# Optimization experiments

Hardware: AMD Instinct MI355X
Metric: run time of the kernel (lower is better)

The kernel has to match this reference:

```python
import jax, jax.numpy as jnp
import numpy as np

SIDES, LAYERS, NH = 2, 2, 2
DEPTH, B = 7, 8
NPT = (3 ** DEPTH - 1) // 2  # 1093 nodes per perfect ternary tree
N = B * NPT                  # 8744
E, H = 256, 512
NUM_USERS, NUM_POIS, NUM_CATS, NUM_COOS, TMAX = 2000, 5000, 300, 50, 600
FUSE = NUM_POIS + NUM_CATS + NUM_COOS


def setup_inputs() -> dict:
    key = jax.random.key(0)
    cnt = [0]
    def nk():
        cnt[0] += 1
        return jax.random.fold_in(key, cnt[0])
    def rn(*s):
        return jax.random.normal(nk(), s, jnp.float32) * 0.02
    inp = dict(
        user_ids=jax.random.randint(nk(), (SIDES, N), 0, NUM_USERS, jnp.int32),
        feat_ids=jax.random.randint(nk(), (SIDES, N), 0, FUSE, jnp.int32),
        time_ids=jax.random.randint(nk(), (SIDES, N), 0, TMAX, jnp.int32),
        mask=jnp.ones((SIDES, N), jnp.int32),
        depth=DEPTH, n_trees=B,
        user_emb=rn(SIDES, NUM_USERS, 128), fuse_emb=rn(SIDES, FUSE, 128),
        time_pe=rn(SIDES, TMAX, E),
        Wf=rn(SIDES, H, E), bf=jnp.zeros((SIDES, H)),
        Wiou=rn(SIDES, 3 * H, E), Uiou=rn(SIDES, 3 * H, 3 * H), biou=jnp.zeros((SIDES, 3 * H)),
        attn_in_w=rn(SIDES, LAYERS, 3 * H, H), attn_in_b=jnp.zeros((SIDES, LAYERS, 3 * H)),
        attn_out_w=rn(SIDES, LAYERS, H, H), attn_out_b=jnp.zeros((SIDES, LAYERS, H)),
        ff1_w=rn(SIDES, LAYERS, H, H), ff1_b=jnp.zeros((SIDES, LAYERS, H)),
        ff2_w=rn(SIDES, LAYERS, H, H), ff2_b=jnp.zeros((SIDES, LAYERS, H)),
        ln1_w=jnp.ones((SIDES, LAYERS, H)), ln1_b=jnp.zeros((SIDES, LAYERS, H)),
        ln2_w=jnp.ones((SIDES, LAYERS, H)), ln2_b=jnp.zeros((SIDES, LAYERS, H)),
        dec_poi_w=rn(SIDES, NUM_POIS, H), dec_poi_b=jnp.zeros((SIDES, NUM_POIS)),
        dec_cat_w=rn(SIDES, NUM_CATS, H), dec_cat_b=jnp.zeros((SIDES, NUM_CATS)),
        dec_coo_w=rn(SIDES, NUM_COOS, H), dec_coo_b=jnp.zeros((SIDES, NUM_COOS)),
        cat2poi_w=rn(SIDES, NUM_POIS, NUM_CATS), cat2poi_b=jnp.zeros((SIDES, NUM_POIS)),
        coo2poi_w=rn(SIDES, NUM_POIS, NUM_COOS), coo2poi_b=jnp.zeros((SIDES, NUM_POIS)),
        mtl=jnp.ones((SIDES, 3)),
        c0=(jax.random.uniform(nk(), (SIDES, N, H), jnp.float32) * 2.0 - 1.0) * 0.025,
    )
    return inp


def _ln(x, w, b, eps=1e-5):
    m = x.mean(-1, keepdims=True)
    v = ((x - m) ** 2).mean(-1, keepdims=True)
    return (x - m) / jnp.sqrt(v + eps) * w + b


def _mha(x, iw, ib, ow, ob):
    M, S, Hd = x.shape
    q, k, v = jnp.split(x @ iw.T + ib, 3, -1)
    hd = Hd // NH
    def rs(t):
        return t.reshape(M, S, NH, hd).transpose(0, 2, 1, 3)
    q, k, v = rs(q), rs(k), rs(v)
    att = jax.nn.softmax((q * (hd ** -0.5)) @ k.transpose(0, 1, 3, 2), -1)
    o = (att @ v).transpose(0, 2, 1, 3).reshape(M, S, Hd)
    return o @ ow.T + ob


def _enc(x, iw, ib, ow, ob, f1w, f1b, f2w, f2b, l1w, l1b, l2w, l2b):
    # post-norm TransformerEncoderLayer, relu, eval mode (no dropout)
    x = _ln(x + _mha(x, iw, ib, ow, ob), l1w, l1b)
    return _ln(x + (jax.nn.relu(x @ f1w.T + f1b) @ f2w.T + f2b), l2w, l2b)


def _forward(user_ids, feat_ids, time_ids, mask, depth, n_trees,
             user_emb, fuse_emb, time_pe, Wf, bf, Wiou, Uiou, biou,
             attn_in_w, attn_in_b, attn_out_w, attn_out_b,
             ff1_w, ff1_b, ff2_w, ff2_b, ln1_w, ln1_b, ln2_w, ln2_b,
             dec_poi_w, dec_poi_b, dec_cat_w, dec_cat_b, dec_coo_w, dec_coo_b,
             cat2poi_w, cat2poi_b, coo2poi_w, coo2poi_b, mtl, c0):
    Hd = Wf.shape[1]
    npt = (3 ** depth - 1) // 2
    Bt = n_trees
    offs = [(3 ** l - 1) // 2 for l in range(depth)]
    outs = []
    for s in range(SIDES):
        m = mask[s]
        uid, fid, tid = user_ids[s] * m, feat_ids[s] * m, time_ids[s] * m
        emb = jnp.concatenate([user_emb[s][uid], fuse_emb[s][fid]], -1) + 0.5 * time_pe[s][tid]
        mf = m.astype(emb.dtype)[:, None]
        x = (emb * mf).reshape(Bt, npt, -1)              # masked node features
        iou0 = ((emb @ Wiou[s].T) * mf).reshape(Bt, npt, 3 * Hd)  # leaf iou init
        c0s = c0[s].reshape(Bt, npt, Hd)
        h = jnp.zeros((Bt, npt, Hd), emb.dtype)
        c = jnp.zeros((Bt, npt, Hd), emb.dtype)
        for l in range(depth - 1, -1, -1):  # bottom-up topo propagation, level-major layout
            st, n = offs[l], 3 ** l
            if l == depth - 1:  # leaves: no reduce, apply with initial iou and c
                iou = iou0[:, st:st + n]
                cpre = c0s[:, st:st + n]
            else:
                cs = offs[l + 1]
                hch = h[:, cs:cs + 3 * n].reshape(Bt * n, 3, Hd)   # mailbox h_child
                cch = c[:, cs:cs + 3 * n].reshape(Bt, n, 3, Hd)    # mailbox c_child
                z = hch
                for L in range(LAYERS):
                    z = _enc(z, attn_in_w[s, L], attn_in_b[s, L], attn_out_w[s, L], attn_out_b[s, L],
                             ff1_w[s, L], ff1_b[s, L], ff2_w[s, L], ff2_b[s, L],
                             ln1_w[s, L], ln1_b[s, L], ln2_w[s, L], ln2_b[s, L])
                hc = z.reshape(Bt, n, 3 * Hd)
                xl = x[:, st:st + n]
                Wx = xl @ Wf[s].T
                f = jax.nn.sigmoid(jnp.concatenate([Wx] * 3, -1) + hc + jnp.tile(bf[s], 3))
                iou = xl @ Wiou[s].T + hc @ Uiou[s].T + biou[s]
                cpre = jnp.sum(f.reshape(Bt, n, 3, Hd) * cch, axis=2)
            i, o, u = jnp.split(iou, 3, -1)
            cn = jax.nn.sigmoid(i) * jnp.tanh(u) + cpre
            hn = jax.nn.sigmoid(o) * jnp.tanh(cn)
            h = h.at[:, st:st + n].set(hn)
            c = c.at[:, st:st + n].set(cn)
        hN = h.reshape(-1, Hd)
        poi = hN @ dec_poi_w[s].T + dec_poi_b[s]
        cat = hN @ dec_cat_w[s].T + dec_cat_b[s]
        coo = hN @ dec_coo_w[s].T + dec_coo_b[s]
        p = mtl[s]
        poi_mt = (0.5 * jnp.exp(-p[0]) * poi + p[0]
                  + 0.5 * jnp.exp(-p[1]) * (cat @ cat2poi_w[s].T + cat2poi_b[s]) + p[1]
                  + 0.5 * jnp.exp(-p[2]) * (coo @ coo2poi_w[s].T + coo2poi_b[s]) + p[2])
        outs += [poi_mt, cat, coo]
    return tuple(outs)


def reference(user_ids, feat_ids, time_ids, mask, depth, n_trees,
              user_emb, fuse_emb, time_pe, Wf, bf, Wiou, Uiou, biou,
              attn_in_w, attn_in_b, attn_out_w, attn_out_b,
              ff1_w, ff1_b, ff2_w, ff2_b, ln1_w, ln1_b, ln2_w, ln2_b,
              dec_poi_w, dec_poi_b, dec_cat_w, dec_cat_b, dec_coo_w, dec_coo_b,
              cat2poi_w, cat2poi_b, coo2poi_w, coo2poi_b, mtl, c0):
    return _forward(user_ids, feat_ids, time_ids, mask, depth, n_trees,
                    user_emb, fuse_emb, time_pe, Wf, bf, Wiou, Uiou, biou,
                    attn_in_w, attn_in_b, attn_out_w, attn_out_b,
                    ff1_w, ff1_b, ff2_w, ff2_b, ln1_w, ln1_b, ln2_w, ln2_b,
                    dec_poi_w, dec_poi_b, dec_cat_w, dec_cat_b, dec_coo_w, dec_coo_b,
                    cat2poi_w, cat2poi_b, coo2poi_w, coo2poi_b, mtl, c0)
```

## Files before the change

### kernel.cpp

```cpp
#include <hip/hip_runtime.h>
#include <math.h>

#define SIDES 2
#define LAYERS 2
#define NTREE 8
#define NPT 1093
#define NN (NTREE*NPT)
#define EE 256
#define HH 512
#define NUSERS 2000
#define NPOI 5000
#define NCAT 300
#define NCOO 50
#define FUSEN 5350
#define TMAXN 600
#define TOKMAX 5832
#define PARMAX 1944

constexpr long OUT_S   = 46780400L;
constexpr long CAT_OFF = 43720000L;
constexpr long COO_OFF = 46343200L;

constexpr long H_S    = (long)NN*HH;
constexpr long X_S    = (long)NN*EE;
constexpr long Z_S    = (long)TOKMAX*HH;
constexpr long QKV_S  = (long)TOKMAX*3*HH;
constexpr long WXI_S  = (long)PARMAX*2048;
constexpr long WEFF_S = (long)NPOI*HH;

typedef __attribute__((ext_vector_type(8))) short  bf16x8;
typedef __attribute__((ext_vector_type(8))) ushort u16x8;
typedef __attribute__((ext_vector_type(4))) ushort u16x4;
typedef __attribute__((ext_vector_type(4))) float  f32x4;

__device__ __forceinline__ float sigm(float x){ return 1.f/(1.f+expf(-x)); }
__device__ __forceinline__ ushort f2b(float f){
  union { float f; unsigned u; } v; v.f = f;
  return (ushort)((v.u + 0x7fffu + ((v.u >> 16) & 1u)) >> 16);
}
__device__ __forceinline__ float b2f(ushort u){
  union { unsigned u; float f; } v; v.u = (unsigned)u << 16; return v.f;
}

__global__ void mcvt_k(ushort* d0, const float* s0, long n0,
                       ushort* d1, const float* s1, long n1,
                       ushort* d2, const float* s2, long n2,
                       ushort* d3, const float* s3, long n3,
                       ushort* d4, const float* s4, long n4,
                       ushort* d5, const float* s5, long n5){
  long g4 = (long)blockIdx.x*blockDim.x + threadIdx.x;
  long i = g4*4;
  ushort* d; const float* s; long off;
  if      (i < n0){ d=d0; s=s0; off=i; }
  else if ((i-=n0) < n1){ d=d1; s=s1; off=i; }
  else if ((i-=n1) < n2){ d=d2; s=s2; off=i; }
  else if ((i-=n2) < n3){ d=d3; s=s3; off=i; }
  else if ((i-=n3) < n4){ d=d4; s=s4; off=i; }
  else if ((i-=n4) < n5){ d=d5; s=s5; off=i; }
  else return;
  f32x4 v = *(const f32x4*)(s + off);
  *(u16x4*)(d + off) = (u16x4){f2b(v[0]), f2b(v[1]), f2b(v[2]), f2b(v[3])};
}

__global__ void wcomb_k(ushort* __restrict__ dst, const float* __restrict__ Wf,
                        const float* __restrict__ Wiou, const float* __restrict__ Uiou){
  int s = blockIdx.z; int row = blockIdx.x; int col = blockIdx.y*256 + threadIdx.x;
  float v;
  if (row < 512) v = (col < 256) ? Wf[((long)s*512 + row)*256 + col] : 0.f;
  else {
    int r = row - 512;
    v = (col < 256) ? Wiou[((long)s*1536 + r)*256 + col]
                    : Uiou[((long)s*1536 + r)*1536 + (col-256)];
  }
  dst[(long)s*2048*1792 + (long)row*1792 + col] = f2b(v);
}

__global__ void bcomb_k(float* __restrict__ dst, const float* __restrict__ biou){
  int s = blockIdx.z; int c = blockIdx.x*256 + threadIdx.x;
  dst[(long)s*2048 + c] = (c < 512) ? 0.f : biou[(long)s*1536 + (c-512)];
}

__global__ void padcvt_k(ushort* __restrict__ dst, const float* __restrict__ src,
                         int rows, int scols, int dcols){
  int s = blockIdx.z; int r = blockIdx.x; int c = blockIdx.y*256 + threadIdx.x;
  if (c >= dcols) return;
  float v = (c < scols) ? src[((long)s*rows + r)*scols + c] : 0.f;
  dst[((long)s*rows + r)*dcols + c] = f2b(v);
}

__global__ void tpcvt_k(ushort* __restrict__ dst, const float* __restrict__ src,
                        int srows, int dcols){
  int s = blockIdx.z; int h = blockIdx.x; int c = threadIdx.x;
  float v = (c < srows) ? src[((long)s*srows + c)*512 + h] : 0.f;
  dst[((long)s*512 + h)*dcols + c] = f2b(v);
}

__global__ void weffinit_k(ushort* __restrict__ dst, const float* __restrict__ poi_w,
                           const float* __restrict__ mtl){
  int s = blockIdx.z;
  long i = ((long)blockIdx.x*blockDim.x + threadIdx.x)*4;
  float a0 = 0.5f*expf(-mtl[(long)s*3]);
  f32x4 v = *(const f32x4*)(poi_w + (long)s*WEFF_S + i);
  *(u16x4*)(dst + (long)s*WEFF_S + i) =
      (u16x4){f2b(a0*v[0]), f2b(a0*v[1]), f2b(a0*v[2]), f2b(a0*v[3])};
}

__global__ void beff_k(float* __restrict__ beff, const float* __restrict__ poi_b,
                       const float* __restrict__ cat_b, const float* __restrict__ c2p_w,
                       const float* __restrict__ c2p_b, const float* __restrict__ coo_b,
                       const float* __restrict__ o2p_w, const float* __restrict__ o2p_b,
                       const float* __restrict__ mtl){
  int s = blockIdx.z;
  int n = blockIdx.x*blockDim.x + threadIdx.x;
  if (n >= NPOI) return;
  const float* mt = mtl + (long)s*3;
  float a0 = 0.5f*expf(-mt[0]), a1 = 0.5f*expf(-mt[1]), a2 = 0.5f*expf(-mt[2]);
  float acc1 = 0.f, acc2 = 0.f;
  for (int c = 0; c < NCAT; c++)
    acc1 += cat_b[(long)s*NCAT + c] * c2p_w[((long)s*NPOI + n)*NCAT + c];
  for (int c = 0; c < NCOO; c++)
    acc2 += coo_b[(long)s*NCOO + c] * o2p_w[((long)s*NPOI + n)*NCOO + c];
  beff[(long)s*NPOI + n] = a0*poi_b[(long)s*NPOI + n]
      + a1*(acc1 + c2p_b[(long)s*NPOI + n]) + a2*(acc2 + o2p_b[(long)s*NPOI + n])
      + mt[0] + mt[1] + mt[2];
}

__global__ void embed_k(const int* __restrict__ uid, const int* __restrict__ fid,
                        const int* __restrict__ tid, const int* __restrict__ mask,
                        const float* __restrict__ uemb, const float* __restrict__ femb,
                        const float* __restrict__ tpe, ushort* __restrict__ X){
  int s = blockIdx.z; long i = blockIdx.x; int d = threadIdx.x;
  int m = mask[(long)s*NN + i];
  int u = uid[(long)s*NN + i]*m, f = fid[(long)s*NN + i]*m, t = tid[(long)s*NN + i]*m;
  float e = (d < 128) ? uemb[((long)s*NUSERS + u)*128 + d]
                      : femb[((long)s*FUSEN + f)*128 + (d-128)];
  e += 0.5f * tpe[((long)s*TMAXN + t)*256 + d];
  X[(long)s*X_S + i*EE + d] = f2b(e * (float)m);
}

template<int MODE, bool OBF>
__global__ void __launch_bounds__(256)
mgemm_k(const ushort* __restrict__ A1, long lda1, long sA1,
        const ushort* __restrict__ A2, long lda2, long sA2,
        int kSplit, int mapN, int mapOff,
        const ushort* __restrict__ Wt, long ldw, long sW,
        const float* __restrict__ bias, long sB,
        void* __restrict__ Cv, long ldc, long sC,
        int M, int Nc, int K, int nbx,
        const float* __restrict__ mtl, int mtlIdx){
  int s = blockIdx.z;
  A1 += (long)s*sA1; A2 += (long)s*sA2; Wt += (long)s*sW;
  if (bias) bias += (long)s*sB;

  int flat = blockIdx.x, nwg = gridDim.x;
  int xcd = flat & 7, q = nwg >> 3, r8 = nwg & 7;
  int nf = (xcd < r8 ? xcd*(q+1) : r8*(q+1) + (xcd - r8)*q) + (flat >> 3);
  int bx = nf % nbx, by = nf / nbx;
  int m0 = by*128, n0 = bx*128;

  __shared__ ushort As[128*64];
  __shared__ ushort Ws[128*64];

  int tid = threadIdx.x;
  int lane = tid & 63, wave = tid >> 6;
  int wr = wave >> 1, wc = wave & 1;
  int fr = lane & 15, kc = lane >> 4;

  int baseRow = tid >> 3;
  int c16 = tid & 7;
  int col8 = c16*8;
  int swz = (baseRow & 7) << 4;

  long gA1[4], gA2[4], gW[4];
  int wbyte[4];
  #pragma unroll
  for (int c = 0; c < 4; c++){
    int row = baseRow + c*32;
    int ra = m0 + row; if (ra > M-1) ra = M-1;
    gA2[c] = ra;
    if (mapN > 0){ int tr = ra / mapN; gA1[c] = (long)(tr*NPT + mapOff + (ra - tr*mapN)); }
    else gA1[c] = ra;
    int rw = n0 + row; if (rw > Nc-1) rw = Nc-1;
    gW[c] = rw;
    wbyte[c] = row*128 + ((c16*16) ^ swz);
  }

  u16x8 rA[4], rW[4];
  {
    bool u1 = (0 < kSplit);
    const ushort* asrc = u1 ? A1 : A2;
    long ld = u1 ? lda1 : lda2;
    const long* g = u1 ? gA1 : gA2;
    #pragma unroll
    for (int c = 0; c < 4; c++){
      rA[c] = *(const u16x8*)(asrc + g[c]*ld + col8);
      rW[c] = *(const u16x8*)(Wt + gW[c]*ldw + col8);
    }
  }

  f32x4 acc[4][4];
  #pragma unroll
  for (int i = 0; i < 4; i++)
    #pragma unroll
    for (int j = 0; j < 4; j++) acc[i][j] = (f32x4){0.f,0.f,0.f,0.f};

  for (int k0 = 0; k0 < K; k0 += 64){
    #pragma unroll
    for (int c = 0; c < 4; c++){
      *(u16x8*)((char*)As + wbyte[c]) = rA[c];
      *(u16x8*)((char*)Ws + wbyte[c]) = rW[c];
    }
    __syncthreads();
    int kn = k0 + 64;
    if (kn < K){
      bool u1 = (kn < kSplit);
      const ushort* asrc = u1 ? A1 : A2;
      long ld = u1 ? lda1 : lda2;
      const long* g = u1 ? gA1 : gA2;
      long colb = u1 ? (long)kn : (long)(kn - kSplit);
      #pragma unroll
      for (int c = 0; c < 4; c++){
        rA[c] = *(const u16x8*)(asrc + g[c]*ld + colb + col8);
        rW[c] = *(const u16x8*)(Wt + gW[c]*ldw + kn + col8);
      }
    }
    #pragma unroll
    for (int h = 0; h < 2; h++){
      bf16x8 af[4], bw[4];
      #pragma unroll
      for (int i = 0; i < 4; i++){
        int row = wr*64 + i*16 + fr;
        int byo = row*128 + ((h*64 + kc*16) ^ ((row & 7) << 4));
        af[i] = *(const bf16x8*)((const char*)As + byo);
      }
      #pragma unroll
      for (int j = 0; j < 4; j++){
        int row = wc*64 + j*16 + fr;
        int byo = row*128 + ((h*64 + kc*16) ^ ((row & 7) << 4));
        bw[j] = *(const bf16x8*)((const char*)Ws + byo);
      }
      #pragma unroll
      for (int i = 0; i < 4; i++)
        #pragma unroll
        for (int j = 0; j < 4; j++)
          acc[i][j] = __builtin_amdgcn_mfma_f32_16x16x32_bf16(bw[j], af[i], acc[i][j], 0, 0, 0);
    }
    __syncthreads();
  }

  float alpha = 1.f;
  if (MODE == 4) alpha = 0.5f*expf(-mtl[(long)s*3 + mtlIdx]);
  int ccol = lane & 15, cr4 = (lane >> 4)*4;
  bool vecN = ((Nc & 3) == 0);
  float* Cf = (float*)Cv + (long)s*sC;
  ushort* Cb = (ushort*)Cv + (long)s*sC;
  #pragma unroll
  for (int i = 0; i < 4; i++){
    int gm = m0 + wr*64 + i*16 + ccol;
    if (gm >= M) continue;
    long rowoff = (long)gm*ldc;
    #pragma unroll
    for (int j = 0; j < 4; j++){
      int gn0 = n0 + wc*64 + j*16 + cr4;
      if (gn0 >= Nc) continue;
      f32x4 v = acc[i][j];
      if (MODE != 4 && bias){ f32x4 bv = *(const f32x4*)&bias[gn0]; v += bv; }
      if (MODE == 1){ v = (f32x4){fmaxf(v[0],0.f),fmaxf(v[1],0.f),fmaxf(v[2],0.f),fmaxf(v[3],0.f)}; }
      if (OBF){
        u16x4* cp = (u16x4*)&Cb[rowoff + gn0];
        if (MODE == 4){
          u16x4 o = *cp;
          *cp = (u16x4){f2b(b2f(o[0]) + alpha*v[0]), f2b(b2f(o[1]) + alpha*v[1]),
                        f2b(b2f(o[2]) + alpha*v[2]), f2b(b2f(o[3]) + alpha*v[3])};
        } else {
          *cp = (u16x4){f2b(v[0]), f2b(v[1]), f2b(v[2]), f2b(v[3])};
        }
      } else {
        if (vecN){
          f32x4* cp = (f32x4*)&Cf[rowoff + gn0];
          if (MODE == 4){ f32x4 o = *cp; *cp = o + alpha*v; }
          else *cp = v;
        } else {
          #pragma unroll
          for (int r = 0; r < 4; r++){
            int gn = gn0 + r; if (gn >= Nc) continue;
            if (MODE == 4) Cf[rowoff + gn] += alpha*v[r];
            else Cf[rowoff + gn] = v[r];
          }
        }
      }
    }
  }
}

__global__ void attn_k(const ushort* __restrict__ qkv, ushort* __restrict__ o){
  int s = blockIdx.z, m = blockIdx.x, h = blockIdx.y;
  const ushort* base = qkv + (long)s*QKV_S + (long)m*3*1536 + (long)h*256;
  int t = threadIdx.x;
  float q[3], k[3], v[3];
  #pragma unroll
  for (int i = 0; i < 3; i++){
    q[i] = b2f(base[(long)i*1536 + t]);
    k[i] = b2f(base[(long)i*1536 + 512 + t]);
    v[i] = b2f(base[(long)i*1536 + 1024 + t]);
  }
  __shared__ float sm[4];
  __shared__ float att[9];
  #pragma unroll
  for (int i = 0; i < 3; i++)
    #pragma unroll
    for (int j = 0; j < 3; j++){
      float p = q[i]*k[j];
      for (int off = 32; off; off >>= 1) p += __shfl_down(p, off);
      __syncthreads();
      if ((t & 63) == 0) sm[t >> 6] = p;
      __syncthreads();
      if (t == 0) att[i*3 + j] = (sm[0]+sm[1]+sm[2]+sm[3]) * 0.0625f;
    }
  __syncthreads();
  if (t < 3){
    float a = att[t*3], b = att[t*3+1], c = att[t*3+2];
    float mx = fmaxf(a, fmaxf(b, c));
    a = expf(a-mx); b = expf(b-mx); c = expf(c-mx);
    float inv = 1.f/(a+b+c);
    att[t*3] = a*inv; att[t*3+1] = b*inv; att[t*3+2] = c*inv;
  }
  __syncthreads();
  ushort* ob = o + (long)s*Z_S + (long)m*3*512 + (long)h*256;
  #pragma unroll
  for (int i = 0; i < 3; i++)
    ob[(long)i*512 + t] = f2b(att[i*3]*v[0] + att[i*3+1]*v[1] + att[i*3+2]*v[2]);
}

__global__ void add_ln_k(ushort* __restrict__ zout, long sZ,
                         const ushort* __restrict__ res, long sR, int mapN, int mapOff,
                         const ushort* __restrict__ tb, long sT,
                         const float* __restrict__ w, const float* __restrict__ b, long wstr){
  int s = blockIdx.z; int r = blockIdx.x;
  int g = r;
  if (mapN > 0){ int tr = r / mapN; g = tr*NPT + mapOff + (r - tr*mapN); }
  const ushort* rr = res + (long)s*sR + (long)g*HH;
  const ushort* tr_ = tb + (long)s*sT + (long)r*HH;
  const float* wr = w + (long)s*wstr;
  const float* br = b + (long)s*wstr;
  int d0 = threadIdx.x, d1 = threadIdx.x + 256;
  float x0 = b2f(rr[d0]) + b2f(tr_[d0]), x1 = b2f(rr[d1]) + b2f(tr_[d1]);
  __shared__ float sm[4];
  float tsum = x0 + x1;
  for (int off = 32; off; off >>= 1) tsum += __shfl_down(tsum, off);
  if ((threadIdx.x & 63) == 0) sm[threadIdx.x >> 6] = tsum;
  __syncthreads();
  float mean = (sm[0]+sm[1]+sm[2]+sm[3]) * (1.f/512.f);
  float e0 = x0 - mean, e1 = x1 - mean;
  float vs = e0*e0 + e1*e1;
  __syncthreads();
  for (int off = 32; off; off >>= 1) vs += __shfl_down(vs, off);
  if ((threadIdx.x & 63) == 0) sm[threadIdx.x >> 6] = vs;
  __syncthreads();
  float var = (sm[0]+sm[1]+sm[2]+sm[3]) * (1.f/512.f);
  float inv = 1.f/sqrtf(var + 1e-5f);
  ushort* zr = zout + (long)s*sZ + (long)r*HH;
  zr[d0] = f2b(e0*inv*wr[d0] + br[d0]);
  zr[d1] = f2b(e1*inv*wr[d1] + br[d1]);
}

__global__ void leaf_k(const ushort* __restrict__ iou, const float* __restrict__ c0,
                       ushort* __restrict__ hbuf, float* __restrict__ cbuf){
  int s = blockIdx.z, p = blockIdx.x;
  int tree = p / 729, j = p - tree*729;
  long row = (long)(tree*NPT + 364 + j)*HH;
  const ushort* iour = iou + (long)s*QKV_S + (long)p*1536;
  const float* c0r = c0 + (long)s*H_S + row;
  for (int d = threadIdx.x; d < HH; d += 256){
    float cn = sigm(b2f(iour[d])) * tanhf(b2f(iour[1024 + d])) + c0r[d];
    float hn = sigm(b2f(iour[512 + d])) * tanhf(cn);
    hbuf[(long)s*H_S + row + d] = f2b(hn);
    cbuf[(long)s*H_S + row + d] = cn;
  }
}

__global__ void combine_k(const ushort* __restrict__ wxiou, const ushort* __restrict__ z,
                          const float* __restrict__ bfv, const float* __restrict__ cbuf,
                          ushort* __restrict__ hbuf, float* __restrict__ cout,
                          int n, int st, int cs){
  int s = blockIdx.z, p = blockIdx.x;
  int tree = p / n, j = p - tree*n;
  const ushort* wr_ = wxiou + (long)s*WXI_S + (long)p*2048;
  const ushort* zr  = z + (long)s*Z_S + (long)p*1536;
  const float* bfr  = bfv + (long)s*HH;
  const float* cch  = cbuf + (long)s*H_S + (long)(tree*NPT + cs + 3*j)*HH;
  long orow = (long)s*H_S + (long)(tree*NPT + st + j)*HH;
  for (int d = threadIdx.x; d < HH; d += 256){
    float wv = b2f(wr_[d]) + bfr[d];
    float cpre = 0.f;
    #pragma unroll
    for (int ch = 0; ch < 3; ch++){
      float fg = sigm(wv + b2f(zr[ch*512 + d]));
      cpre += fg * cch[ch*512 + d];
    }
    float iv = b2f(wr_[512 + d]), ov = b2f(wr_[1024 + d]), uv = b2f(wr_[1536 + d]);
    float cn = sigm(iv)*tanhf(uv) + cpre;
    float hn = sigm(ov)*tanhf(cn);
    hbuf[orow + d] = f2b(hn);
    cout[orow + d] = cn;
  }
}

#define GEMM(MODE, OBF, A1, LDA1, SA1, A2, LDA2, SA2, KSPL, MAPN, MAPOFF, WT, LDW, SW, \
             BI, SB, CC, LDC, SC, M, NC, K)                                            \
  do { int nbx_ = ((NC)+127)/128, nby_ = ((M)+127)/128;                                \
    mgemm_k<MODE, OBF><<<dim3(nbx_*nby_, 1, SIDES), 256, 0, stream>>>(                 \
      A1, LDA1, SA1, A2, LDA2, SA2, KSPL, MAPN, MAPOFF, WT, LDW, SW, BI, SB,           \
      CC, LDC, SC, M, NC, K, nbx_, mtl, 0); } while(0)
#define GEMM4(OBF, A1, LDA1, SA1, WT, LDW, SW, CC, LDC, SC, M, NC, K, IDX)             \
  do { int nbx_ = ((NC)+127)/128, nby_ = ((M)+127)/128;                                \
    mgemm_k<4, OBF><<<dim3(nbx_*nby_, 1, SIDES), 256, 0, stream>>>(                    \
      A1, LDA1, SA1, A1, LDA1, SA1, K, 0, 0, WT, LDW, SW, (const float*)nullptr, 0L,   \
      CC, LDC, SC, M, NC, K, nbx_, mtl, IDX); } while(0)

extern "C" void kernel_launch(void* const* d_in, const int* in_sizes, int n_in,
                              void* d_out, int out_size, void* d_ws, size_t ws_size,
                              hipStream_t stream){
  (void)in_sizes; (void)n_in; (void)out_size; (void)ws_size;
  const int*   user_ids  = (const int*)d_in[0];
  const int*   feat_ids  = (const int*)d_in[1];
  const int*   time_ids  = (const int*)d_in[2];
  const int*   mask      = (const int*)d_in[3];
  const float* user_emb  = (const float*)d_in[6];
  const float* fuse_emb  = (const float*)d_in[7];
  const float* time_pe   = (const float*)d_in[8];
  const float* Wf        = (const float*)d_in[9];
  const float* bf        = (const float*)d_in[10];
  const float* Wiou      = (const float*)d_in[11];
  const float* Uiou      = (const float*)d_in[12];
  const float* biou      = (const float*)d_in[13];
  const float* attn_in_w = (const float*)d_in[14];
  const float* attn_in_b = (const float*)d_in[15];
  const float* attn_out_w= (const float*)d_in[16];
  const float* attn_out_b= (const float*)d_in[17];
  const float* ff1_w     = (const float*)d_in[18];
  const float* ff1_b     = (const float*)d_in[19];
  const float* ff2_w     = (const float*)d_in[20];
  const float* ff2_b     = (const float*)d_in[21];
  const float* ln1_w     = (const float*)d_in[22];
  const float* ln1_b     = (const float*)d_in[23];
  const float* ln2_w     = (const float*)d_in[24];
  const float* ln2_b     = (const float*)d_in[25];
  const float* dec_poi_w = (const float*)d_in[26];
  const float* dec_poi_b = (const float*)d_in[27];
  const float* dec_cat_w = (const float*)d_in[28];
  const float* dec_cat_b = (const float*)d_in[29];
  const float* dec_coo_w = (const float*)d_in[30];
  const float* dec_coo_b = (const float*)d_in[31];
  const float* cat2poi_w = (const float*)d_in[32];
  const float* cat2poi_b = (const float*)d_in[33];
  const float* coo2poi_w = (const float*)d_in[34];
  const float* coo2poi_b = (const float*)d_in[35];
  const float* mtl       = (const float*)d_in[36];
  const float* c0        = (const float*)d_in[37];

  float* out = (float*)d_out;

  ushort* wsu = (ushort*)d_ws;
  ushort* Hb    = wsu;
  ushort* ainW  = Hb    + 2*H_S;
  ushort* aoutW = ainW  + (long)2*2*1536*512;
  ushort* f1W   = aoutW + (long)2*2*512*512;
  ushort* f2W   = f1W   + (long)2*2*512*512;
  ushort* wcomb = f2W   + (long)2*2*512*512;
  ushort* dcatW = wcomb + (long)2*2048*1792;
  ushort* dcooW = dcatW + (long)2*300*512;
  ushort* weffB = dcooW + (long)2*50*512;
  float*  bcomb = (float*)(weffB + (long)2*WEFF_S);
  float*  beff  = bcomb + 2*2048;

  float*  Cb   = out + OUT_S;
  ushort* osu  = (ushort*)(Cb + 2*H_S);
  ushort* QKV  = osu;
  ushort* Zb   = QKV  + 2*QKV_S;
  ushort* TMP  = Zb   + 2*Z_S;
  ushort* WXI  = TMP  + 2*Z_S;
  ushort* Xb   = WXI  + 2*WXI_S;
  ushort* c2pB = Xb   + 2*X_S;
  ushort* o2pB = c2pB + (long)2*5000*320;
  ushort* dctT = o2pB + (long)2*5000*64;
  ushort* dcoT = dctT + (long)2*512*320;

  {
    long n0 = (long)2*2*1536*512, n1 = (long)2*2*512*512, n2 = n1, n3 = n1;
    long n4 = (long)2*300*512, n5 = (long)2*50*512;
    long tot4 = (n0+n1+n2+n3+n4+n5)/4;
    mcvt_k<<<dim3((tot4+255)/256), 256, 0, stream>>>(
        ainW, attn_in_w, n0, aoutW, attn_out_w, n1, f1W, ff1_w, n2,
        f2W, ff2_w, n3, dcatW, dec_cat_w, n4, dcooW, dec_coo_w, n5);
  }
  wcomb_k<<<dim3(2048, 7, SIDES), 256, 0, stream>>>(wcomb, Wf, Wiou, Uiou);
  bcomb_k<<<dim3(8, 1, SIDES), 256, 0, stream>>>(bcomb, biou);
  padcvt_k<<<dim3(5000, 2, SIDES), 256, 0, stream>>>(c2pB, cat2poi_w, 5000, 300, 320);
  padcvt_k<<<dim3(5000, 1, SIDES), 256, 0, stream>>>(o2pB, coo2poi_w, 5000, 50, 64);
  tpcvt_k<<<dim3(512, 1, SIDES), 320, 0, stream>>>(dctT, dec_cat_w, 300, 320);
  tpcvt_k<<<dim3(512, 1, SIDES), 64, 0, stream>>>(dcoT, dec_coo_w, 50, 64);
  weffinit_k<<<dim3(2500, 1, SIDES), 256, 0, stream>>>(weffB, dec_poi_w, mtl);
  beff_k<<<dim3(20, 1, SIDES), 256, 0, stream>>>(beff, dec_poi_b, dec_cat_b,
       cat2poi_w, cat2poi_b, dec_coo_b, coo2poi_w, coo2poi_b, mtl);

  embed_k<<<dim3(NN, 1, SIDES), 256, 0, stream>>>(user_ids, feat_ids, time_ids, mask,
                                                  user_emb, fuse_emb, time_pe, Xb);

  GEMM(0, true, Xb, 256L, X_S, Xb, 256L, X_S, 256, 729, 364,
       wcomb + (long)512*1792, 1792L, (long)2048*1792,
       (const float*)nullptr, 0L, QKV, 1536L, QKV_S, 5832, 1536, 256);
  leaf_k<<<dim3(5832, 1, SIDES), 256, 0, stream>>>(QKV, c0, Hb, Cb);

  const int p3[7]   = {1,3,9,27,81,243,729};
  const int offs[7] = {0,1,4,13,40,121,364};

  for (int l = 5; l >= 0; l--){
    int n = p3[l], st = offs[l], cs = offs[l+1];
    int P = NTREE*n, T = 3*P;
    for (int L = 0; L < LAYERS; L++){
      const ushort* zin = (L == 0) ? Hb : Zb;
      long zld = 512, zs = (L == 0) ? H_S : Z_S;
      int mN = (L == 0) ? 3*n : 0, mO = (L == 0) ? cs : 0;
      GEMM(0, true, zin, zld, zs, zin, zld, zs, 512, mN, mO,
           ainW + (long)L*1536*512, 512L, (long)2*1536*512,
           attn_in_b + (long)L*1536, (long)LAYERS*1536, QKV, 1536L, QKV_S, T, 1536, 512);
      attn_k<<<dim3(P, 2, SIDES), 256, 0, stream>>>(QKV, TMP);
      GEMM(0, true, TMP, 512L, Z_S, TMP, 512L, Z_S, 512, 0, 0,
           aoutW + (long)L*512*512, 512L, (long)2*512*512,
           attn_out_b + (long)L*512, (long)LAYERS*512, QKV, 512L, QKV_S, T, 512, 512);
      add_ln_k<<<dim3(T, 1, SIDES), 256, 0, stream>>>(Zb, Z_S, zin, zs, mN, mO,
           QKV, QKV_S, ln1_w + (long)L*512, ln1_b + (long)L*512, (long)LAYERS*512);
      GEMM(1, true, Zb, 512L, Z_S, Zb, 512L, Z_S, 512, 0, 0,
           f1W + (long)L*512*512, 512L, (long)2*512*512,
           ff1_b + (long)L*512, (long)LAYERS*512, TMP, 512L, Z_S, T, 512, 512);
      GEMM(0, true, TMP, 512L, Z_S, TMP, 512L, Z_S, 512, 0, 0,
           f2W + (long)L*512*512, 512L, (long)2*512*512,
           ff2_b + (long)L*512, (long)LAYERS*512, QKV, 512L, QKV_S, T, 512, 512);
      add_ln_k<<<dim3(T, 1, SIDES), 256, 0, stream>>>(Zb, Z_S, Zb, Z_S, 0, 0,
           QKV, QKV_S, ln2_w + (long)L*512, ln2_b + (long)L*512, (long)LAYERS*512);
    }
    GEMM(0, true, Xb, 256L, X_S, Zb, 1536L, Z_S, 256, n, st,
         wcomb, 1792L, (long)2048*1792, bcomb, 2048L, WXI, 2048L, WXI_S, P, 2048, 1792);
    combine_k<<<dim3(P, 1, SIDES), 256, 0, stream>>>(WXI, Zb, bf, Cb, Hb, Cb, n, st, cs);
  }

  GEMM(0, false, Hb, 512L, H_S, Hb, 512L, H_S, 512, 0, 0,
       dcatW, 512L, (long)NCAT*512, dec_cat_b, (long)NCAT,
       out + CAT_OFF, (long)NCAT, OUT_S, NN, NCAT, 512);
  GEMM(0, false, Hb, 512L, H_S, Hb, 512L, H_S, 512, 0, 0,
       dcooW, 512L, (long)NCOO*512, dec_coo_b, (long)NCOO,
       out + COO_OFF, (long)NCOO, OUT_S, NN, NCOO, 512);

  GEMM4(true, c2pB, 320L, (long)5000*320, dctT, 320L, (long)512*320,
        weffB, 512L, WEFF_S, 5000, 512, 320, 1);
  GEMM4(true, o2pB, 64L, (long)5000*64, dcoT, 64L, (long)512*64,
        weffB, 512L, WEFF_S, 5000, 512, 64, 2);

  GEMM(0, false, Hb, 512L, H_S, Hb, 512L, H_S, 512, 0, 0,
       weffB, 512L, WEFF_S, beff, (long)NPOI,
       out, (long)NPOI, OUT_S, NN, NPOI, 512);
}
```

Measured before the change: 1.652 ms.

## Fuse prep kernels into one launch and make attention and LayerNorm wave-per-row

All weight conversion, padding, transpose, bias and embedding prep kernels are merged into a single prep_k launch, with blocks dispatched by index range. attn_k now gives each 64-lane wave one (sequence, head) pair with vectorized loads and xor-shuffle reductions, removing shared memory and __syncthreads. add_ln_k now handles one row per wave with 8-element vector loads and stores, so it launches four times fewer blocks. The aim is to cut launch overhead and synchronization in small kernels that run many times; the merged prep kernel has branchy block dispatch and some loops that leave lanes unevenly used.

```diff
diff --git a/kernel.cpp b/kernel.cpp
--- a/kernel.cpp
+++ b/kernel.cpp
@@ -42,100 +42,133 @@
   union { unsigned u; float f; } v; v.u = (unsigned)u << 16; return v.f;
 }
 
-__global__ void mcvt_k(ushort* d0, const float* s0, long n0,
-                       ushort* d1, const float* s1, long n1,
-                       ushort* d2, const float* s2, long n2,
-                       ushort* d3, const float* s3, long n3,
-                       ushort* d4, const float* s4, long n4,
-                       ushort* d5, const float* s5, long n5){
-  long g4 = (long)blockIdx.x*blockDim.x + threadIdx.x;
-  long i = g4*4;
-  ushort* d; const float* s; long off;
-  if      (i < n0){ d=d0; s=s0; off=i; }
-  else if ((i-=n0) < n1){ d=d1; s=s1; off=i; }
-  else if ((i-=n1) < n2){ d=d2; s=s2; off=i; }
-  else if ((i-=n2) < n3){ d=d3; s=s3; off=i; }
-  else if ((i-=n3) < n4){ d=d4; s=s4; off=i; }
-  else if ((i-=n4) < n5){ d=d5; s=s5; off=i; }
-  else return;
-  f32x4 v = *(const f32x4*)(s + off);
-  *(u16x4*)(d + off) = (u16x4){f2b(v[0]), f2b(v[1]), f2b(v[2]), f2b(v[3])};
-}
-
-__global__ void wcomb_k(ushort* __restrict__ dst, const float* __restrict__ Wf,
-                        const float* __restrict__ Wiou, const float* __restrict__ Uiou){
-  int s = blockIdx.z; int row = blockIdx.x; int col = blockIdx.y*256 + threadIdx.x;
-  float v;
-  if (row < 512) v = (col < 256) ? Wf[((long)s*512 + row)*256 + col] : 0.f;
-  else {
-    int r = row - 512;
-    v = (col < 256) ? Wiou[((long)s*1536 + r)*256 + col]
-                    : Uiou[((long)s*1536 + r)*1536 + (col-256)];
-  }
-  dst[(long)s*2048*1792 + (long)row*1792 + col] = f2b(v);
-}
-
-__global__ void bcomb_k(float* __restrict__ dst, const float* __restrict__ biou){
-  int s = blockIdx.z; int c = blockIdx.x*256 + threadIdx.x;
-  dst[(long)s*2048 + c] = (c < 512) ? 0.f : biou[(long)s*1536 + (c-512)];
-}
-
-__global__ void padcvt_k(ushort* __restrict__ dst, const float* __restrict__ src,
-                         int rows, int scols, int dcols){
-  int s = blockIdx.z; int r = blockIdx.x; int c = blockIdx.y*256 + threadIdx.x;
-  if (c >= dcols) return;
-  float v = (c < scols) ? src[((long)s*rows + r)*scols + c] : 0.f;
-  dst[((long)s*rows + r)*dcols + c] = f2b(v);
-}
-
-__global__ void tpcvt_k(ushort* __restrict__ dst, const float* __restrict__ src,
-                        int srows, int dcols){
-  int s = blockIdx.z; int h = blockIdx.x; int c = threadIdx.x;
-  float v = (c < srows) ? src[((long)s*srows + c)*512 + h] : 0.f;
-  dst[((long)s*512 + h)*dcols + c] = f2b(v);
-}
-
-__global__ void weffinit_k(ushort* __restrict__ dst, const float* __restrict__ poi_w,
-                           const float* __restrict__ mtl){
-  int s = blockIdx.z;
-  long i = ((long)blockIdx.x*blockDim.x + threadIdx.x)*4;
-  float a0 = 0.5f*expf(-mtl[(long)s*3]);
-  f32x4 v = *(const f32x4*)(poi_w + (long)s*WEFF_S + i);
-  *(u16x4*)(dst + (long)s*WEFF_S + i) =
-      (u16x4){f2b(a0*v[0]), f2b(a0*v[1]), f2b(a0*v[2]), f2b(a0*v[3])};
-}
-
-__global__ void beff_k(float* __restrict__ beff, const float* __restrict__ poi_b,
-                       const float* __restrict__ cat_b, const float* __restrict__ c2p_w,
-                       const float* __restrict__ c2p_b, const float* __restrict__ coo_b,
-                       const float* __restrict__ o2p_w, const float* __restrict__ o2p_b,
-                       const float* __restrict__ mtl){
-  int s = blockIdx.z;
-  int n = blockIdx.x*blockDim.x + threadIdx.x;
-  if (n >= NPOI) return;
-  const float* mt = mtl + (long)s*3;
-  float a0 = 0.5f*expf(-mt[0]), a1 = 0.5f*expf(-mt[1]), a2 = 0.5f*expf(-mt[2]);
-  float acc1 = 0.f, acc2 = 0.f;
-  for (int c = 0; c < NCAT; c++)
-    acc1 += cat_b[(long)s*NCAT + c] * c2p_w[((long)s*NPOI + n)*NCAT + c];
-  for (int c = 0; c < NCOO; c++)
-    acc2 += coo_b[(long)s*NCOO + c] * o2p_w[((long)s*NPOI + n)*NCOO + c];
-  beff[(long)s*NPOI + n] = a0*poi_b[(long)s*NPOI + n]
-      + a1*(acc1 + c2p_b[(long)s*NPOI + n]) + a2*(acc2 + o2p_b[(long)s*NPOI + n])
-      + mt[0] + mt[1] + mt[2];
-}
-
-__global__ void embed_k(const int* __restrict__ uid, const int* __restrict__ fid,
-                        const int* __restrict__ tid, const int* __restrict__ mask,
-                        const float* __restrict__ uemb, const float* __restrict__ femb,
-                        const float* __restrict__ tpe, ushort* __restrict__ X){
-  int s = blockIdx.z; long i = blockIdx.x; int d = threadIdx.x;
-  int m = mask[(long)s*NN + i];
-  int u = uid[(long)s*NN + i]*m, f = fid[(long)s*NN + i]*m, t = tid[(long)s*NN + i]*m;
-  float e = (d < 128) ? uemb[((long)s*NUSERS + u)*128 + d]
-                      : femb[((long)s*FUSEN + f)*128 + (d-128)];
-  e += 0.5f * tpe[((long)s*TMAXN + t)*256 + d];
-  X[(long)s*X_S + i*EE + d] = f2b(e * (float)m);
+constexpr int PB_EMB  = 2*NN;
+constexpr int PB_MCVT = 6494;
+constexpr int PB_WCOMB= 2*2048;
+constexpr int PB_BCOMB= 16;
+constexpr int PB_POI  = 2*5000;
+constexpr int PB_TP   = 2*512;
+constexpr int PB_WEI  = 2*2500;
+constexpr int PB_BEF  = 40;
+constexpr int PB_TOT  = PB_EMB+PB_MCVT+PB_WCOMB+PB_BCOMB+PB_POI+PB_TP+PB_WEI+PB_BEF;
+
+__global__ void __launch_bounds__(256) prep_k(
+    const int* __restrict__ uid, const int* __restrict__ fid,
+    const int* __restrict__ tids, const int* __restrict__ mask,
+    const float* __restrict__ uemb, const float* __restrict__ femb,
+    const float* __restrict__ tpe, ushort* __restrict__ X,
+    ushort* ainW, const float* attn_in_w, ushort* aoutW, const float* attn_out_w,
+    ushort* f1W, const float* ff1_w, ushort* f2W, const float* ff2_w,
+    ushort* dcatW, const float* dec_cat_w, ushort* dcooW, const float* dec_coo_w,
+    ushort* wcomb, const float* Wf, const float* Wiou, const float* Uiou,
+    float* bcomb, const float* biou,
+    ushort* c2pB, const float* cat2poi_w, ushort* o2pB, const float* coo2poi_w,
+    ushort* dctT, ushort* dcoT,
+    ushort* weffB, const float* dec_poi_w, const float* mtl,
+    float* beff, const float* dec_poi_b, const float* dec_cat_b,
+    const float* cat2poi_b, const float* dec_coo_b, const float* coo2poi_b){
+  int b = blockIdx.x;
+  int tid = threadIdx.x;
+  if (b < PB_EMB){
+    int s = b / NN; long i = b - s*NN; int d = tid;
+    int m = mask[(long)s*NN + i];
+    int u = uid[(long)s*NN + i]*m, f = fid[(long)s*NN + i]*m, t = tids[(long)s*NN + i]*m;
+    float e = (d < 128) ? uemb[((long)s*NUSERS + u)*128 + d]
+                        : femb[((long)s*FUSEN + f)*128 + (d-128)];
+    e += 0.5f * tpe[((long)s*TMAXN + t)*256 + d];
+    X[(long)s*X_S + i*EE + d] = f2b(e * (float)m);
+    return;
+  }
+  b -= PB_EMB;
+  if (b < PB_MCVT){
+    const long n0 = 3145728, n1 = 1048576, n2 = 1048576, n3 = 1048576,
+               n4 = 307200, n5 = 51200;
+    long i = ((long)b*256 + tid)*4;
+    ushort* d; const float* s; long off;
+    if      (i < n0){ d=ainW;  s=attn_in_w;  off=i; }
+    else if ((i-=n0) < n1){ d=aoutW; s=attn_out_w; off=i; }
+    else if ((i-=n1) < n2){ d=f1W;  s=ff1_w;  off=i; }
+    else if ((i-=n2) < n3){ d=f2W;  s=ff2_w;  off=i; }
+    else if ((i-=n3) < n4){ d=dcatW; s=dec_cat_w; off=i; }
+    else if ((i-=n4) < n5){ d=dcooW; s=dec_coo_w; off=i; }
+    else return;
+    f32x4 v = *(const f32x4*)(s + off);
+    *(u16x4*)(d + off) = (u16x4){f2b(v[0]), f2b(v[1]), f2b(v[2]), f2b(v[3])};
+    return;
+  }
+  b -= PB_MCVT;
+  if (b < PB_WCOMB){
+    int s = b >> 11; int row = b & 2047;
+    ushort* dst = wcomb + (long)s*2048*1792 + (long)row*1792;
+    for (int col = tid; col < 1792; col += 256){
+      float v;
+      if (row < 512) v = (col < 256) ? Wf[((long)s*512 + row)*256 + col] : 0.f;
+      else {
+        int r = row - 512;
+        v = (col < 256) ? Wiou[((long)s*1536 + r)*256 + col]
+                        : Uiou[((long)s*1536 + r)*1536 + (col-256)];
+      }
+      dst[col] = f2b(v);
+    }
+    return;
+  }
+  b -= PB_WCOMB;
+  if (b < PB_BCOMB){
+    int s = b >> 3; int c = (b & 7)*256 + tid;
+    bcomb[(long)s*2048 + c] = (c < 512) ? 0.f : biou[(long)s*1536 + (c-512)];
+    return;
+  }
+  b -= PB_BCOMB;
+  if (b < PB_POI){
+    int s = b / 5000; int r = b - s*5000;
+    for (int c = tid; c < 320; c += 256){
+      float v = (c < 300) ? cat2poi_w[((long)s*5000 + r)*300 + c] : 0.f;
+      c2pB[((long)s*5000 + r)*320 + c] = f2b(v);
+    }
+    if (tid < 64){
+      float v = (tid < 50) ? coo2poi_w[((long)s*5000 + r)*50 + tid] : 0.f;
+      o2pB[((long)s*5000 + r)*64 + tid] = f2b(v);
+    }
+    return;
+  }
+  b -= PB_POI;
+  if (b < PB_TP){
+    int s = b >> 9; int h = b & 511;
+    for (int c = tid; c < 320; c += 256){
+      float v = (c < 300) ? dec_cat_w[((long)s*300 + c)*512 + h] : 0.f;
+      dctT[((long)s*512 + h)*320 + c] = f2b(v);
+    }
+    if (tid < 64){
+      float v = (tid < 50) ? dec_coo_w[((long)s*50 + tid)*512 + h] : 0.f;
+      dcoT[((long)s*512 + h)*64 + tid] = f2b(v);
+    }
+    return;
+  }
+  b -= PB_TP;
+  if (b < PB_WEI){
+    int s = b / 2500; int blk = b - s*2500;
+    long i = ((long)blk*256 + tid)*4;
+    float a0 = 0.5f*expf(-mtl[(long)s*3]);
+    f32x4 v = *(const f32x4*)(dec_poi_w + (long)s*WEFF_S + i);
+    *(u16x4*)(weffB + (long)s*WEFF_S + i) =
+        (u16x4){f2b(a0*v[0]), f2b(a0*v[1]), f2b(a0*v[2]), f2b(a0*v[3])};
+    return;
+  }
+  b -= PB_WEI;
+  {
+    int s = b / 20; int n = (b - s*20)*256 + tid;
+    if (n >= NPOI) return;
+    const float* mt = mtl + (long)s*3;
+    float a0 = 0.5f*expf(-mt[0]), a1 = 0.5f*expf(-mt[1]), a2 = 0.5f*expf(-mt[2]);
+    float acc1 = 0.f, acc2 = 0.f;
+    for (int c = 0; c < NCAT; c++)
+      acc1 += dec_cat_b[(long)s*NCAT + c] * cat2poi_w[((long)s*NPOI + n)*NCAT + c];
+    for (int c = 0; c < NCOO; c++)
+      acc2 += dec_coo_b[(long)s*NCOO + c] * coo2poi_w[((long)s*NPOI + n)*NCOO + c];
+    beff[(long)s*NPOI + n] = a0*dec_poi_b[(long)s*NPOI + n]
+        + a1*(acc1 + cat2poi_b[(long)s*NPOI + n]) + a2*(acc2 + coo2poi_b[(long)s*NPOI + n])
+        + mt[0] + mt[1] + mt[2];
+  }
 }
 
 template<int MODE, bool OBF>
@@ -293,75 +326,93 @@
   }
 }
 
-__global__ void attn_k(const ushort* __restrict__ qkv, ushort* __restrict__ o){
-  int s = blockIdx.z, m = blockIdx.x, h = blockIdx.y;
-  const ushort* base = qkv + (long)s*QKV_S + (long)m*3*1536 + (long)h*256;
-  int t = threadIdx.x;
-  float q[3], k[3], v[3];
+__global__ void __launch_bounds__(256) attn_k(const ushort* __restrict__ qkv,
+                                              ushort* __restrict__ o){
+  int s = blockIdx.z;
+  int w = threadIdx.x >> 6, lane = threadIdx.x & 63;
+  int seq = blockIdx.x*2 + (w >> 1);
+  int h = w & 1;
+  const ushort* base = qkv + (long)s*QKV_S + (long)seq*3*1536 + h*256 + lane*4;
+  float q[3][4], k[3][4], v[3][4];
   #pragma unroll
   for (int i = 0; i < 3; i++){
-    q[i] = b2f(base[(long)i*1536 + t]);
-    k[i] = b2f(base[(long)i*1536 + 512 + t]);
-    v[i] = b2f(base[(long)i*1536 + 1024 + t]);
-  }
-  __shared__ float sm[4];
-  __shared__ float att[9];
+    u16x4 tq = *(const u16x4*)(base + (long)i*1536);
+    u16x4 tk = *(const u16x4*)(base + (long)i*1536 + 512);
+    u16x4 tv = *(const u16x4*)(base + (long)i*1536 + 1024);
+    #pragma unroll
+    for (int e = 0; e < 4; e++){ q[i][e]=b2f(tq[e]); k[i][e]=b2f(tk[e]); v[i][e]=b2f(tv[e]); }
+  }
+  float p[9];
   #pragma unroll
   for (int i = 0; i < 3; i++)
     #pragma unroll
     for (int j = 0; j < 3; j++){
-      float p = q[i]*k[j];
-      for (int off = 32; off; off >>= 1) p += __shfl_down(p, off);
-      __syncthreads();
-      if ((t & 63) == 0) sm[t >> 6] = p;
-      __syncthreads();
-      if (t == 0) att[i*3 + j] = (sm[0]+sm[1]+sm[2]+sm[3]) * 0.0625f;
-    }
-  __syncthreads();
-  if (t < 3){
-    float a = att[t*3], b = att[t*3+1], c = att[t*3+2];
-    float mx = fmaxf(a, fmaxf(b, c));
-    a = expf(a-mx); b = expf(b-mx); c = expf(c-mx);
-    float inv = 1.f/(a+b+c);
-    att[t*3] = a*inv; att[t*3+1] = b*inv; att[t*3+2] = c*inv;
-  }
-  __syncthreads();
-  ushort* ob = o + (long)s*Z_S + (long)m*3*512 + (long)h*256;
-  #pragma unroll
-  for (int i = 0; i < 3; i++)
-    ob[(long)i*512 + t] = f2b(att[i*3]*v[0] + att[i*3+1]*v[1] + att[i*3+2]*v[2]);
-}
-
-__global__ void add_ln_k(ushort* __restrict__ zout, long sZ,
+      float acc = 0.f;
+      #pragma unroll
+      for (int e = 0; e < 4; e++) acc += q[i][e]*k[j][e];
+      p[i*3+j] = acc;
+    }
+  #pragma unroll
+  for (int m = 1; m < 64; m <<= 1)
+    #pragma unroll
+    for (int t = 0; t < 9; t++) p[t] += __shfl_xor(p[t], m);
+  float att[9];
+  #pragma unroll
+  for (int i = 0; i < 3; i++){
+    float a = p[i*3]*0.0625f, bb = p[i*3+1]*0.0625f, c = p[i*3+2]*0.0625f;
+    float mx = fmaxf(a, fmaxf(bb, c));
+    a = expf(a-mx); bb = expf(bb-mx); c = expf(c-mx);
+    float inv = 1.f/(a+bb+c);
+    att[i*3] = a*inv; att[i*3+1] = bb*inv; att[i*3+2] = c*inv;
+  }
+  ushort* ob = o + (long)s*Z_S + (long)seq*1536 + h*256 + lane*4;
+  #pragma unroll
+  for (int i = 0; i < 3; i++){
+    u16x4 r;
+    #pragma unroll
+    for (int e = 0; e < 4; e++)
+      r[e] = f2b(att[i*3]*v[0][e] + att[i*3+1]*v[1][e] + att[i*3+2]*v[2][e]);
+    *(u16x4*)(ob + (long)i*512) = r;
+  }
+}
+
+__global__ void __launch_bounds__(256) add_ln_k(ushort* __restrict__ zout, long sZ,
                          const ushort* __restrict__ res, long sR, int mapN, int mapOff,
                          const ushort* __restrict__ tb, long sT,
-                         const float* __restrict__ w, const float* __restrict__ b, long wstr){
-  int s = blockIdx.z; int r = blockIdx.x;
+                         const float* __restrict__ w, const float* __restrict__ b,
+                         long wstr){
+  int s = blockIdx.z;
+  int wv = threadIdx.x >> 6, lane = threadIdx.x & 63;
+  int r = blockIdx.x*4 + wv;
   int g = r;
   if (mapN > 0){ int tr = r / mapN; g = tr*NPT + mapOff + (r - tr*mapN); }
-  const ushort* rr = res + (long)s*sR + (long)g*HH;
-  const ushort* tr_ = tb + (long)s*sT + (long)r*HH;
-  const float* wr = w + (long)s*wstr;
-  const float* br = b + (long)s*wstr;
-  int d0 = threadIdx.x, d1 = threadIdx.x + 256;
-  float x0 = b2f(rr[d0]) + b2f(tr_[d0]), x1 = b2f(rr[d1]) + b2f(tr_[d1]);
-  __shared__ float sm[4];
-  float tsum = x0 + x1;
-  for (int off = 32; off; off >>= 1) tsum += __shfl_down(tsum, off);
-  if ((threadIdx.x & 63) == 0) sm[threadIdx.x >> 6] = tsum;
-  __syncthreads();
-  float mean = (sm[0]+sm[1]+sm[2]+sm[3]) * (1.f/512.f);
-  float e0 = x0 - mean, e1 = x1 - mean;
-  float vs = e0*e0 + e1*e1;
-  __syncthreads();
-  for (int off = 32; off; off >>= 1) vs += __shfl_down(vs, off);
-  if ((threadIdx.x & 63) == 0) sm[threadIdx.x >> 6] = vs;
-  __syncthreads();
-  float var = (sm[0]+sm[1]+sm[2]+sm[3]) * (1.f/512.f);
-  float inv = 1.f/sqrtf(var + 1e-5f);
-  ushort* zr = zout + (long)s*sZ + (long)r*HH;
-  zr[d0] = f2b(e0*inv*wr[d0] + br[d0]);
-  zr[d1] = f2b(e1*inv*wr[d1] + br[d1]);
+  int d0 = lane*8;
+  u16x8 rr = *(const u16x8*)(res + (long)s*sR + (long)g*HH + d0);
+  u16x8 tt = *(const u16x8*)(tb  + (long)s*sT + (long)r*HH + d0);
+  float x[8];
+  float sum = 0.f;
+  #pragma unroll
+  for (int e = 0; e < 8; e++){ x[e] = b2f(rr[e]) + b2f(tt[e]); sum += x[e]; }
+  #pragma unroll
+  for (int m = 1; m < 64; m <<= 1) sum += __shfl_xor(sum, m);
+  float mean = sum * (1.f/512.f);
+  float vs = 0.f;
+  #pragma unroll
+  for (int e = 0; e < 8; e++){ float d = x[e]-mean; vs += d*d; }
+  #pragma unroll
+  for (int m = 1; m < 64; m <<= 1) vs += __shfl_xor(vs, m);
+  float inv = 1.f/sqrtf(vs*(1.f/512.f) + 1e-5f);
+  const float* wr_ = w + (long)s*wstr + d0;
+  const float* br_ = b + (long)s*wstr + d0;
+  f32x4 w0 = *(const f32x4*)wr_, w1 = *(const f32x4*)(wr_+4);
+  f32x4 b0 = *(const f32x4*)br_, b1 = *(const f32x4*)(br_+4);
+  u16x8 ov;
+  #pragma unroll
+  for (int e = 0; e < 4; e++){
+    ov[e]   = f2b((x[e]-mean)*inv*w0[e] + b0[e]);
+    ov[e+4] = f2b((x[e+4]-mean)*inv*w1[e] + b1[e]);
+  }
+  *(u16x8*)(zout + (long)s*sZ + (long)r*HH + d0) = ov;
 }
 
 __global__ void leaf_k(const ushort* __restrict__ iou, const float* __restrict__ c0,
@@ -486,26 +537,14 @@
   ushort* dctT = o2pB + (long)2*5000*64;
   ushort* dcoT = dctT + (long)2*512*320;
 
-  {
-    long n0 = (long)2*2*1536*512, n1 = (long)2*2*512*512, n2 = n1, n3 = n1;
-    long n4 = (long)2*300*512, n5 = (long)2*50*512;
-    long tot4 = (n0+n1+n2+n3+n4+n5)/4;
-    mcvt_k<<<dim3((tot4+255)/256), 256, 0, stream>>>(
-        ainW, attn_in_w, n0, aoutW, attn_out_w, n1, f1W, ff1_w, n2,
-        f2W, ff2_w, n3, dcatW, dec_cat_w, n4, dcooW, dec_coo_w, n5);
-  }
-  wcomb_k<<<dim3(2048, 7, SIDES), 256, 0, stream>>>(wcomb, Wf, Wiou, Uiou);
-  bcomb_k<<<dim3(8, 1, SIDES), 256, 0, stream>>>(bcomb, biou);
-  padcvt_k<<<dim3(5000, 2, SIDES), 256, 0, stream>>>(c2pB, cat2poi_w, 5000, 300, 320);
-  padcvt_k<<<dim3(5000, 1, SIDES), 256, 0, stream>>>(o2pB, coo2poi_w, 5000, 50, 64);
-  tpcvt_k<<<dim3(512, 1, SIDES), 320, 0, stream>>>(dctT, dec_cat_w, 300, 320);
-  tpcvt_k<<<dim3(512, 1, SIDES), 64, 0, stream>>>(dcoT, dec_coo_w, 50, 64);
-  weffinit_k<<<dim3(2500, 1, SIDES), 256, 0, stream>>>(weffB, dec_poi_w, mtl);
-  beff_k<<<dim3(20, 1, SIDES), 256, 0, stream>>>(beff, dec_poi_b, dec_cat_b,
-       cat2poi_w, cat2poi_b, dec_coo_b, coo2poi_w, coo2poi_b, mtl);
-
-  embed_k<<<dim3(NN, 1, SIDES), 256, 0, stream>>>(user_ids, feat_ids, time_ids, mask,
-                                                  user_emb, fuse_emb, time_pe, Xb);
+  prep_k<<<dim3(PB_TOT), 256, 0, stream>>>(
+      user_ids, feat_ids, time_ids, mask, user_emb, fuse_emb, time_pe, Xb,
+      ainW, attn_in_w, aoutW, attn_out_w, f1W, ff1_w, f2W, ff2_w,
+      dcatW, dec_cat_w, dcooW, dec_coo_w,
+      wcomb, Wf, Wiou, Uiou, bcomb, biou,
+      c2pB, cat2poi_w, o2pB, coo2poi_w, dctT, dcoT,
+      weffB, dec_poi_w, mtl,
+      beff, dec_poi_b, dec_cat_b, cat2poi_b, dec_coo_b, coo2poi_b);
 
   GEMM(0, true, Xb, 256L, X_S, Xb, 256L, X_S, 256, 729, 364,
        wcomb + (long)512*1792, 1792L, (long)2048*1792,
@@ -525,11 +564,11 @@
       GEMM(0, true, zin, zld, zs, zin, zld, zs, 512, mN, mO,
            ainW + (long)L*1536*512, 512L, (long)2*1536*512,
            attn_in_b + (long)L*1536, (long)LAYERS*1536, QKV, 1536L, QKV_S, T, 1536, 512);
-      attn_k<<<dim3(P, 2, SIDES), 256, 0, stream>>>(QKV, TMP);
+      attn_k<<<dim3(P/2, 1, SIDES), 256, 0, stream>>>(QKV, TMP);
       GEMM(0, true, TMP, 512L, Z_S, TMP, 512L, Z_S, 512, 0, 0,
            aoutW + (long)L*512*512, 512L, (long)2*512*512,
            attn_out_b + (long)L*512, (long)LAYERS*512, QKV, 512L, QKV_S, T, 512, 512);
-      add_ln_k<<<dim3(T, 1, SIDES), 256, 0, stream>>>(Zb, Z_S, zin, zs, mN, mO,
+      add_ln_k<<<dim3(T/4, 1, SIDES), 256, 0, stream>>>(Zb, Z_S, zin, zs, mN, mO,
            QKV, QKV_S, ln1_w + (long)L*512, ln1_b + (long)L*512, (long)LAYERS*512);
       GEMM(1, true, Zb, 512L, Z_S, Zb, 512L, Z_S, 512, 0, 0,
            f1W + (long)L*512*512, 512L, (long)2*512*512,
@@ -537,7 +576,7 @@
       GEMM(0, true, TMP, 512L, Z_S, TMP, 512L, Z_S, 512, 0, 0,
            f2W + (long)L*512*512, 512L, (long)2*512*512,
            ff2_b + (long)L*512, (long)LAYERS*512, QKV, 512L, QKV_S, T, 512, 512);
-      add_ln_k<<<dim3(T, 1, SIDES), 256, 0, stream>>>(Zb, Z_S, Zb, Z_S, 0, 0,
+      add_ln_k<<<dim3(T/4, 1, SIDES), 256, 0, stream>>>(Zb, Z_S, Zb, Z_S, 0, 0,
            QKV, QKV_S, ln2_w + (long)L*512, ln2_b + (long)L*512, (long)LAYERS*512);
     }
     GEMM(0, true, Xb, 256L, X_S, Zb, 1536L, Z_S, 256, n, st,
```

New measurement: 1.560 ms. 5.6% less time.
